# Performance work log

Measured on AMD Instinct MI355X. Metric: run time of the kernel, lower is better.

Reference implementation:

```python
import jax, jax.numpy as jnp
import numpy as np

N, E, D, R, L = 50000, 800000, 128, 4, 2


def setup_inputs() -> dict:
    key = jax.random.key(0)
    ks = jax.random.split(key, 6)
    x = jax.random.normal(ks[0], (N, D), dtype=jnp.float32)
    edge_index = jax.random.randint(ks[1], (2, E), 0, N, dtype=jnp.int64)
    edge_type = jax.random.randint(ks[2], (E,), 0, R, dtype=jnp.int64)
    # per-layer params: relation weights, root weights, biases (fan-in scaled)
    weights = jax.random.normal(ks[3], (L, R, D, D), dtype=jnp.float32) / np.sqrt(D)
    roots = jax.random.normal(ks[4], (L, D, D), dtype=jnp.float32) / np.sqrt(D)
    biases = jnp.zeros((L, D), dtype=jnp.float32)
    return {"x": x, "edge_index": edge_index, "edge_type": edge_type,
            "weights": weights, "roots": roots, "biases": biases}


def _rgcn_conv(x, src, dst, edge_type, weight, root, bias):
    # x: [N, D_in]; weight: [R, D_in, D_out]; root: [D_in, D_out]; bias: [D_out]
    out = x @ root + bias  # root/self transform
    for r in range(R):  # small fixed relation count
        h = x @ weight[r]                                   # [N, D_out]
        m = (edge_type == r).astype(h.dtype)                # [E]
        msgs = h[src] * m[:, None]                          # [E, D_out] gathered messages
        agg = jax.ops.segment_sum(msgs, dst, num_segments=N)
        cnt = jax.ops.segment_sum(m, dst, num_segments=N)
        out = out + agg / jnp.maximum(cnt, 1.0)[:, None]    # per-relation scatter-mean
    return out


def reference(x, edge_index, edge_type, weights, roots, biases):
    src, dst = edge_index[0], edge_index[1]
    h = x
    for i in range(L):
        h = _rgcn_conv(h, src, dst, edge_type, weights[i], roots[i], biases[i])
        if i != L - 1:
            h = jax.nn.relu(h)
    return h
```

## Files before the change

kernel.cpp:

```cpp
#include <hip/hip_runtime.h>


#define N_NODES 50000
#define N_EDGES 800000
#define N_REL 4
#define DIM 128
#define NPAD 50048
#define RN (N_REL * N_NODES)
#define CAP 32

#define HIST_B 3125
#define XCAST_B 3125
#define WPREP_B 640
#define PREP_B (HIST_B + XCAST_B + WPREP_B)

typedef __bf16 bf16x8 __attribute__((ext_vector_type(8)));
typedef float f32x4 __attribute__((ext_vector_type(4)));
typedef float f32x2 __attribute__((ext_vector_type(2)));

__device__ __forceinline__ unsigned short f2bf(float f) {
    unsigned u = __builtin_bit_cast(unsigned, f);
    u += 0x7FFFu + ((u >> 16) & 1u);
    return (unsigned short)(u >> 16);
}

__device__ __forceinline__ unsigned cvt_pk_bf16(float lo, float hi) {
    unsigned r;
    asm("v_cvt_pk_bf16_f32 %0, %1, %2" : "=v"(r) : "v"(lo), "v"(hi));
    return r;
}

__device__ __forceinline__ void pk_add(f32x2& acc, f32x2 v) {
    asm("v_pk_add_f32 %0, %1, %0" : "+v"(acc) : "v"(v));
}

__device__ __forceinline__ void acc_row(f32x2* acc, uint4 d) {
#pragma unroll
    for (int k = 0; k < 4; k++) {
        unsigned dw = (&d.x)[k];
        f32x2 v;
        v[0] = __builtin_bit_cast(float, dw << 16);
        v[1] = __builtin_bit_cast(float, dw & 0xFFFF0000u);
        pk_add(acc[k], v);
    }
}

__device__ __forceinline__ void gload_lds16(const void* g, void* lds) {
    __builtin_amdgcn_global_load_lds(
        (const __attribute__((address_space(1))) void*)g,
        (__attribute__((address_space(3))) void*)lds, 16, 0, 0);
}

__global__ __launch_bounds__(256) void k_prep(const int* __restrict__ et,
                                              const int* __restrict__ dst,
                                              const int* __restrict__ src,
                                              int* __restrict__ cnt,
                                              unsigned short* __restrict__ elist,
                                              const float* __restrict__ X,
                                              unsigned short* __restrict__ Xb,
                                              const float* __restrict__ weights,
                                              const float* __restrict__ roots,
                                              unsigned short* __restrict__ wcatT) {
    const int blk = blockIdx.x, tid = threadIdx.x;
    if (blk < HIST_B) {
        int i = blk * 256 + tid;
        int rn = (dst[i] << 2) | et[i];
        int rk = atomicAdd(&cnt[rn], 1);
        if (rk < CAP) elist[(size_t)rn * CAP + rk] = (unsigned short)src[i];
    } else if (blk < HIST_B + XCAST_B) {
        int i = (blk - HIST_B) * 256 + tid;
        f32x4 a = *(const f32x4*)(X + (size_t)i * 8);
        f32x4 b = *(const f32x4*)(X + (size_t)i * 8 + 4);
        uint4 o;
        o.x = cvt_pk_bf16(a[0], a[1]);
        o.y = cvt_pk_bf16(a[2], a[3]);
        o.z = cvt_pk_bf16(b[0], b[1]);
        o.w = cvt_pk_bf16(b[2], b[3]);
        *(uint4*)(Xb + (size_t)i * 8) = o;
    } else {
        int idx = (blk - HIST_B - XCAST_B) * 256 + tid;
        int k = idx % 640;
        int n = (idx / 640) % 128;
        int l = idx / (640 * 128);
        float v;
        if (k < 128) {
            v = roots[(l * 128 + k) * 128 + n];
        } else {
            int r = (k - 128) >> 7;
            int kk = (k - 128) & 127;
            v = weights[((l * N_REL + r) * 128 + kk) * 128 + n];
        }
        wcatT[idx] = f2bf(v);
    }
}

__global__ __launch_bounds__(256) void k_agg(const unsigned short* __restrict__ Xb,
                                             const int* __restrict__ cnt,
                                             const unsigned short* __restrict__ elist,
                                             unsigned short* __restrict__ xcat) {
    int node = blockIdx.x * 4 + (threadIdx.x >> 6);
    int lane = threadIdx.x & 63;
    const int g = lane >> 4;
    const int t = lane & 15;

    int bucket = (node << 2) | g;
    int c = cnt[bucket];
    c = (c > CAP) ? CAP : c;
    const unsigned short* ep = elist + ((size_t)bucket * CAP);
    uint4 e8 = *(const uint4*)ep;

    int i0 = e8.x & 0xFFFF, i1 = e8.x >> 16;
    int i2 = e8.y & 0xFFFF, i3 = e8.y >> 16;
    int i4 = e8.z & 0xFFFF, i5 = e8.z >> 16;
    int i6 = e8.w & 0xFFFF, i7 = e8.w >> 16;

    const size_t toff = (size_t)(t * 8);
    const uint4 z = {0, 0, 0, 0};
    f32x2 A0[4] = {}, A1[4] = {}, A2[4] = {}, A3[4] = {};

    {
        uint4 d0 = z, d1 = z, d2 = z, d3 = z;
        if (c > 0) d0 = *(const uint4*)(Xb + (size_t)i0 * DIM + toff);
        if (c > 1) d1 = *(const uint4*)(Xb + (size_t)i1 * DIM + toff);
        if (c > 2) d2 = *(const uint4*)(Xb + (size_t)i2 * DIM + toff);
        if (c > 3) d3 = *(const uint4*)(Xb + (size_t)i3 * DIM + toff);
        acc_row(A0, d0); acc_row(A1, d1); acc_row(A2, d2); acc_row(A3, d3);
    }
    if (c > 4) {
        uint4 d0 = z, d1 = z, d2 = z, d3 = z;
        d0 = *(const uint4*)(Xb + (size_t)i4 * DIM + toff);
        if (c > 5) d1 = *(const uint4*)(Xb + (size_t)i5 * DIM + toff);
        if (c > 6) d2 = *(const uint4*)(Xb + (size_t)i6 * DIM + toff);
        if (c > 7) d3 = *(const uint4*)(Xb + (size_t)i7 * DIM + toff);
        acc_row(A0, d0); acc_row(A1, d1); acc_row(A2, d2); acc_row(A3, d3);
    }
    for (int j = 8; j < c; ++j) {
        int s = ep[j];
        uint4 d = *(const uint4*)(Xb + (size_t)s * DIM + toff);
        acc_row(A0, d);
    }
#pragma unroll
    for (int k = 0; k < 4; k++) {
        pk_add(A0[k], A1[k]);
        pk_add(A2[k], A3[k]);
        pk_add(A0[k], A2[k]);
    }

    float inv = 1.0f / fmaxf((float)c, 1.0f);
    uint4 o;
    o.x = cvt_pk_bf16(A0[0][0] * inv, A0[0][1] * inv);
    o.y = cvt_pk_bf16(A0[1][0] * inv, A0[1][1] * inv);
    o.z = cvt_pk_bf16(A0[2][0] * inv, A0[2][1] * inv);
    o.w = cvt_pk_bf16(A0[3][0] * inv, A0[3][1] * inv);
    *(uint4*)(xcat + (size_t)node * 512 + g * 128 + t * 8) = o;
}

__global__ __launch_bounds__(256) void k_gemm(const unsigned short* __restrict__ Xself,
                                              const unsigned short* __restrict__ Xagg,
                                              const unsigned short* __restrict__ Bt,
                                              const float* __restrict__ bias,
                                              void* __restrict__ Yv, int Mout,
                                              int relu, int obf16) {
    __shared__ unsigned short sA[64 * 64];
    __shared__ unsigned short sB[128 * 64];

    const int tid = threadIdx.x;
    const int lane = tid & 63;
    const int wid = tid >> 6;
    const int wm = wid >> 1, wn = wid & 1;
    const int m0 = blockIdx.x * 64;

    f32x4 acc[2][4] = {};

    const char* Bbase = (const char*)Bt;

    for (int kt = 0; kt < 10; ++kt) {
        const char* Asrc;
        size_t rstride;
        if (kt < 2) {
            Asrc = (const char*)Xself + (size_t)m0 * 256 + kt * 128;
            rstride = 256;
        } else {
            Asrc = (const char*)Xagg + (size_t)m0 * 1024 + (kt - 2) * 128;
            rstride = 1024;
        }
#pragma unroll
        for (int i = 0; i < 2; i++) {
            int chunk = i * 256 + tid;
            int row = chunk >> 3, cst = chunk & 7;
            int clog = cst ^ (row & 7);
            gload_lds16(Asrc + (size_t)row * rstride + clog * 16,
                        (char*)sA + (size_t)(chunk - lane) * 16);
        }
#pragma unroll
        for (int i = 0; i < 4; i++) {
            int chunk = i * 256 + tid;
            int row = chunk >> 3, cst = chunk & 7;
            int clog = cst ^ (row & 7);
            gload_lds16(Bbase + (size_t)row * 1280 + kt * 128 + clog * 16,
                        (char*)sB + (size_t)(chunk - lane) * 16);
        }
        __syncthreads();
#pragma unroll
        for (int ki = 0; ki < 2; ki++) {
            bf16x8 a[2], b[4];
#pragma unroll
            for (int mi = 0; mi < 2; mi++) {
                int row = wm * 32 + mi * 16 + (lane & 15);
                int c = ki * 4 + (lane >> 4);
                a[mi] = *(const bf16x8*)((const char*)sA + row * 128 + ((c ^ (row & 7)) << 4));
            }
#pragma unroll
            for (int ni = 0; ni < 4; ni++) {
                int row = wn * 64 + ni * 16 + (lane & 15);
                int c = ki * 4 + (lane >> 4);
                b[ni] = *(const bf16x8*)((const char*)sB + row * 128 + ((c ^ (row & 7)) << 4));
            }
#pragma unroll
            for (int mi = 0; mi < 2; mi++)
#pragma unroll
                for (int ni = 0; ni < 4; ni++)
                    acc[mi][ni] = __builtin_amdgcn_mfma_f32_16x16x32_bf16(a[mi], b[ni], acc[mi][ni], 0, 0, 0);
        }
        __syncthreads();
    }
#pragma unroll
    for (int mi = 0; mi < 2; mi++) {
#pragma unroll
        for (int ni = 0; ni < 4; ni++) {
            int col = wn * 64 + ni * 16 + (lane & 15);
            float bv = bias[col];
#pragma unroll
            for (int q = 0; q < 4; q++) {
                int row = m0 + wm * 32 + mi * 16 + (lane >> 4) * 4 + q;
                if (row < Mout) {
                    float v = acc[mi][ni][q] + bv;
                    if (relu) v = fmaxf(v, 0.f);
                    if (obf16)
                        ((unsigned short*)Yv)[(size_t)row * DIM + col] = f2bf(v);
                    else
                        ((float*)Yv)[(size_t)row * DIM + col] = v;
                }
            }
        }
    }
}

extern "C" void kernel_launch(void* const* d_in, const int* in_sizes, int n_in,
                              void* d_out, int out_size, void* d_ws, size_t ws_size,
                              hipStream_t stream) {
    const float* x = (const float*)d_in[0];
    const int* ei = (const int*)d_in[1];
    const int* et = (const int*)d_in[2];
    const float* weights = (const float*)d_in[3];
    const float* roots = (const float*)d_in[4];
    const float* biases = (const float*)d_in[5];
    float* out = (float*)d_out;

    const int* src = ei;
    const int* dst = ei + N_EDGES;

    int* cnt = (int*)d_ws;
    unsigned short* elist = (unsigned short*)(cnt + 200064);
    unsigned short* wcatT = elist + (size_t)RN * CAP;
    unsigned short* xcat = wcatT + 2 * 128 * 640;
    unsigned short* xb = xcat + (size_t)NPAD * 512;
    unsigned short* hb = xb + (size_t)NPAD * 128;

    hipMemsetAsync(cnt, 0, (size_t)200064 * sizeof(int), stream);

    k_prep<<<PREP_B, 256, 0, stream>>>(et, dst, src, cnt, elist, x, xb, weights, roots, wcatT);

    k_agg<<<N_NODES / 4, 256, 0, stream>>>(xb, cnt, elist, xcat);
    k_gemm<<<NPAD / 64, 256, 0, stream>>>(xb, xcat, wcatT, biases, hb, N_NODES, 1, 1);
    k_agg<<<N_NODES / 4, 256, 0, stream>>>(hb, cnt, elist, xcat);
    k_gemm<<<NPAD / 64, 256, 0, stream>>>(hb, xcat, wcatT + 128 * 640, biases + DIM, out, N_NODES, 0, 0);
}
```

Before: 168.5 us.

## Partition histogram by XCD dst range, widen gather to 8 loads, nontemporal stores

The edge histogram kernel is reorganised so that each block is tied to an XCD (blk&7) and handles only edges whose destination falls in that XCD's node range. Every edge chunk is therefore scanned by 8 blocks, but the atomics and elist writes stay local to one XCD's L2. The aggregation kernel now issues all 8 first-edge gathers up front into 8 independent accumulators, for more memory-level parallelism. The aggregated output and the final fp32 GEMM output use nontemporal stores. The trade-off is that dst is read 8 times over, and the XCD mapping assumes round-robin block dispatch.

```diff
diff --git a/kernel.cpp b/kernel.cpp
--- a/kernel.cpp
+++ b/kernel.cpp
@@ -8,8 +8,11 @@
 #define NPAD 50048
 #define RN (N_REL * N_NODES)
 #define CAP 32
-
-#define HIST_B 3125
+#define NXCD 8
+#define DRANGE 6250
+
+#define HIST_G 391
+#define HIST_B (HIST_G * NXCD)
 #define XCAST_B 3125
 #define WPREP_B 640
 #define PREP_B (HIST_B + XCAST_B + WPREP_B)
@@ -17,6 +20,7 @@
 typedef __bf16 bf16x8 __attribute__((ext_vector_type(8)));
 typedef float f32x4 __attribute__((ext_vector_type(4)));
 typedef float f32x2 __attribute__((ext_vector_type(2)));
+typedef unsigned int u32x4 __attribute__((ext_vector_type(4)));
 
 __device__ __forceinline__ unsigned short f2bf(float f) {
     unsigned u = __builtin_bit_cast(unsigned, f);
@@ -63,20 +67,32 @@
                                               unsigned short* __restrict__ wcatT) {
     const int blk = blockIdx.x, tid = threadIdx.x;
     if (blk < HIST_B) {
-        int i = blk * 256 + tid;
-        int rn = (dst[i] << 2) | et[i];
-        int rk = atomicAdd(&cnt[rn], 1);
-        if (rk < CAP) elist[(size_t)rn * CAP + rk] = (unsigned short)src[i];
+        const int g = blk >> 3;
+        const int x = blk & 7;
+        const int lo = x * DRANGE, hi = lo + DRANGE;
+        const int base = g * 2048;
+#pragma unroll
+        for (int j = 0; j < 8; j++) {
+            int i = base + j * 256 + tid;
+            if (i < N_EDGES) {
+                int d = dst[i];
+                if (d >= lo && d < hi) {
+                    int rn = (d << 2) | et[i];
+                    int rk = atomicAdd(&cnt[rn], 1);
+                    if (rk < CAP) elist[(size_t)rn * CAP + rk] = (unsigned short)src[i];
+                }
+            }
+        }
     } else if (blk < HIST_B + XCAST_B) {
         int i = (blk - HIST_B) * 256 + tid;
         f32x4 a = *(const f32x4*)(X + (size_t)i * 8);
         f32x4 b = *(const f32x4*)(X + (size_t)i * 8 + 4);
-        uint4 o;
+        u32x4 o;
         o.x = cvt_pk_bf16(a[0], a[1]);
         o.y = cvt_pk_bf16(a[2], a[3]);
         o.z = cvt_pk_bf16(b[0], b[1]);
         o.w = cvt_pk_bf16(b[2], b[3]);
-        *(uint4*)(Xb + (size_t)i * 8) = o;
+        *(u32x4*)(Xb + (size_t)i * 8) = o;
     } else {
         int idx = (blk - HIST_B - XCAST_B) * 256 + tid;
         int k = idx % 640;
@@ -117,22 +133,20 @@
     const size_t toff = (size_t)(t * 8);
     const uint4 z = {0, 0, 0, 0};
     f32x2 A0[4] = {}, A1[4] = {}, A2[4] = {}, A3[4] = {};
+    f32x2 A4[4] = {}, A5[4] = {}, A6[4] = {}, A7[4] = {};
 
     {
-        uint4 d0 = z, d1 = z, d2 = z, d3 = z;
+        uint4 d0 = z, d1 = z, d2 = z, d3 = z, d4 = z, d5 = z, d6 = z, d7 = z;
         if (c > 0) d0 = *(const uint4*)(Xb + (size_t)i0 * DIM + toff);
         if (c > 1) d1 = *(const uint4*)(Xb + (size_t)i1 * DIM + toff);
         if (c > 2) d2 = *(const uint4*)(Xb + (size_t)i2 * DIM + toff);
         if (c > 3) d3 = *(const uint4*)(Xb + (size_t)i3 * DIM + toff);
+        if (c > 4) d4 = *(const uint4*)(Xb + (size_t)i4 * DIM + toff);
+        if (c > 5) d5 = *(const uint4*)(Xb + (size_t)i5 * DIM + toff);
+        if (c > 6) d6 = *(const uint4*)(Xb + (size_t)i6 * DIM + toff);
+        if (c > 7) d7 = *(const uint4*)(Xb + (size_t)i7 * DIM + toff);
         acc_row(A0, d0); acc_row(A1, d1); acc_row(A2, d2); acc_row(A3, d3);
-    }
-    if (c > 4) {
-        uint4 d0 = z, d1 = z, d2 = z, d3 = z;
-        d0 = *(const uint4*)(Xb + (size_t)i4 * DIM + toff);
-        if (c > 5) d1 = *(const uint4*)(Xb + (size_t)i5 * DIM + toff);
-        if (c > 6) d2 = *(const uint4*)(Xb + (size_t)i6 * DIM + toff);
-        if (c > 7) d3 = *(const uint4*)(Xb + (size_t)i7 * DIM + toff);
-        acc_row(A0, d0); acc_row(A1, d1); acc_row(A2, d2); acc_row(A3, d3);
+        acc_row(A4, d4); acc_row(A5, d5); acc_row(A6, d6); acc_row(A7, d7);
     }
     for (int j = 8; j < c; ++j) {
         int s = ep[j];
@@ -143,16 +157,20 @@
     for (int k = 0; k < 4; k++) {
         pk_add(A0[k], A1[k]);
         pk_add(A2[k], A3[k]);
+        pk_add(A4[k], A5[k]);
+        pk_add(A6[k], A7[k]);
         pk_add(A0[k], A2[k]);
+        pk_add(A4[k], A6[k]);
+        pk_add(A0[k], A4[k]);
     }
 
     float inv = 1.0f / fmaxf((float)c, 1.0f);
-    uint4 o;
+    u32x4 o;
     o.x = cvt_pk_bf16(A0[0][0] * inv, A0[0][1] * inv);
     o.y = cvt_pk_bf16(A0[1][0] * inv, A0[1][1] * inv);
     o.z = cvt_pk_bf16(A0[2][0] * inv, A0[2][1] * inv);
     o.w = cvt_pk_bf16(A0[3][0] * inv, A0[3][1] * inv);
-    *(uint4*)(xcat + (size_t)node * 512 + g * 128 + t * 8) = o;
+    __builtin_nontemporal_store(o, (u32x4*)(xcat + (size_t)node * 512 + g * 128 + t * 8));
 }
 
 __global__ __launch_bounds__(256) void k_gemm(const unsigned short* __restrict__ Xself,
@@ -236,10 +254,11 @@
                 if (row < Mout) {
                     float v = acc[mi][ni][q] + bv;
                     if (relu) v = fmaxf(v, 0.f);
-                    if (obf16)
+                    if (obf16) {
                         ((unsigned short*)Yv)[(size_t)row * DIM + col] = f2bf(v);
-                    else
-                        ((float*)Yv)[(size_t)row * DIM + col] = v;
+                    } else {
+                        __builtin_nontemporal_store(v, (float*)Yv + (size_t)row * DIM + col);
+                    }
                 }
             }
         }
```

New measurement: 213.3 us. 26.6% more time.

## Pack bucket counts into bytes and split edge lists into dense head plus overflow

Applied to the files above, without the earlier changes.

Edge-bucket counters become 8-bit fields packed four to a 32-bit word, so one atomic word serves all four relations of a node and the memset shrinks fourfold. The per-bucket source lists split into a dense 8-entry head array and a separate 24-entry overflow array. The aggregation kernel then reads a compact 16-byte head per bucket instead of touching a 64-byte-stride list, which cuts scattered memory traffic and the workspace footprint. Counts above 255 would wrap the byte field, so correctness depends on per-bucket degree staying small, which holds for these random inputs.

```diff
diff --git a/kernel.cpp b/kernel.cpp
--- a/kernel.cpp
+++ b/kernel.cpp
@@ -8,6 +8,7 @@
 #define NPAD 50048
 #define RN (N_REL * N_NODES)
 #define CAP 32
+#define OVF 24
 
 #define HIST_B 3125
 #define XCAST_B 3125
@@ -17,6 +18,7 @@
 typedef __bf16 bf16x8 __attribute__((ext_vector_type(8)));
 typedef float f32x4 __attribute__((ext_vector_type(4)));
 typedef float f32x2 __attribute__((ext_vector_type(2)));
+typedef unsigned int u32x4 __attribute__((ext_vector_type(4)));
 
 __device__ __forceinline__ unsigned short f2bf(float f) {
     unsigned u = __builtin_bit_cast(unsigned, f);
@@ -54,8 +56,9 @@
 __global__ __launch_bounds__(256) void k_prep(const int* __restrict__ et,
                                               const int* __restrict__ dst,
                                               const int* __restrict__ src,
-                                              int* __restrict__ cnt,
-                                              unsigned short* __restrict__ elist,
+                                              unsigned* __restrict__ cnt32,
+                                              unsigned short* __restrict__ elist8,
+                                              unsigned short* __restrict__ ovf,
                                               const float* __restrict__ X,
                                               unsigned short* __restrict__ Xb,
                                               const float* __restrict__ weights,
@@ -65,18 +68,24 @@
     if (blk < HIST_B) {
         int i = blk * 256 + tid;
         int rn = (dst[i] << 2) | et[i];
-        int rk = atomicAdd(&cnt[rn], 1);
-        if (rk < CAP) elist[(size_t)rn * CAP + rk] = (unsigned short)src[i];
+        int sh = 8 * (rn & 3);
+        unsigned old = atomicAdd(&cnt32[rn >> 2], 1u << sh);
+        int rk = (old >> sh) & 0xFF;
+        if (rk < 8) {
+            elist8[(size_t)rn * 8 + rk] = (unsigned short)src[i];
+        } else if (rk < CAP) {
+            ovf[(size_t)rn * OVF + (rk - 8)] = (unsigned short)src[i];
+        }
     } else if (blk < HIST_B + XCAST_B) {
         int i = (blk - HIST_B) * 256 + tid;
         f32x4 a = *(const f32x4*)(X + (size_t)i * 8);
         f32x4 b = *(const f32x4*)(X + (size_t)i * 8 + 4);
-        uint4 o;
+        u32x4 o;
         o.x = cvt_pk_bf16(a[0], a[1]);
         o.y = cvt_pk_bf16(a[2], a[3]);
         o.z = cvt_pk_bf16(b[0], b[1]);
         o.w = cvt_pk_bf16(b[2], b[3]);
-        *(uint4*)(Xb + (size_t)i * 8) = o;
+        *(u32x4*)(Xb + (size_t)i * 8) = o;
     } else {
         int idx = (blk - HIST_B - XCAST_B) * 256 + tid;
         int k = idx % 640;
@@ -95,8 +104,9 @@
 }
 
 __global__ __launch_bounds__(256) void k_agg(const unsigned short* __restrict__ Xb,
-                                             const int* __restrict__ cnt,
-                                             const unsigned short* __restrict__ elist,
+                                             const unsigned char* __restrict__ cnt8,
+                                             const unsigned short* __restrict__ elist8,
+                                             const unsigned short* __restrict__ ovf,
                                              unsigned short* __restrict__ xcat) {
     int node = blockIdx.x * 4 + (threadIdx.x >> 6);
     int lane = threadIdx.x & 63;
@@ -104,10 +114,9 @@
     const int t = lane & 15;
 
     int bucket = (node << 2) | g;
-    int c = cnt[bucket];
+    int c = cnt8[bucket];
     c = (c > CAP) ? CAP : c;
-    const unsigned short* ep = elist + ((size_t)bucket * CAP);
-    uint4 e8 = *(const uint4*)ep;
+    uint4 e8 = *(const uint4*)(elist8 + (size_t)bucket * 8);
 
     int i0 = e8.x & 0xFFFF, i1 = e8.x >> 16;
     int i2 = e8.y & 0xFFFF, i3 = e8.y >> 16;
@@ -135,7 +144,7 @@
         acc_row(A0, d0); acc_row(A1, d1); acc_row(A2, d2); acc_row(A3, d3);
     }
     for (int j = 8; j < c; ++j) {
-        int s = ep[j];
+        int s = ovf[(size_t)bucket * OVF + (j - 8)];
         uint4 d = *(const uint4*)(Xb + (size_t)s * DIM + toff);
         acc_row(A0, d);
     }
@@ -147,12 +156,12 @@
     }
 
     float inv = 1.0f / fmaxf((float)c, 1.0f);
-    uint4 o;
+    u32x4 o;
     o.x = cvt_pk_bf16(A0[0][0] * inv, A0[0][1] * inv);
     o.y = cvt_pk_bf16(A0[1][0] * inv, A0[1][1] * inv);
     o.z = cvt_pk_bf16(A0[2][0] * inv, A0[2][1] * inv);
     o.w = cvt_pk_bf16(A0[3][0] * inv, A0[3][1] * inv);
-    *(uint4*)(xcat + (size_t)node * 512 + g * 128 + t * 8) = o;
+    *(u32x4*)(xcat + (size_t)node * 512 + g * 128 + t * 8) = o;
 }
 
 __global__ __launch_bounds__(256) void k_gemm(const unsigned short* __restrict__ Xself,
@@ -260,19 +269,21 @@
     const int* src = ei;
     const int* dst = ei + N_EDGES;
 
-    int* cnt = (int*)d_ws;
-    unsigned short* elist = (unsigned short*)(cnt + 200064);
-    unsigned short* wcatT = elist + (size_t)RN * CAP;
+    unsigned* cnt32 = (unsigned*)d_ws;
+    unsigned short* elist8 = (unsigned short*)(cnt32 + 50016);
+    unsigned short* ovf = elist8 + (size_t)RN * 8;
+    unsigned short* wcatT = ovf + (size_t)RN * OVF;
     unsigned short* xcat = wcatT + 2 * 128 * 640;
     unsigned short* xb = xcat + (size_t)NPAD * 512;
     unsigned short* hb = xb + (size_t)NPAD * 128;
 
-    hipMemsetAsync(cnt, 0, (size_t)200064 * sizeof(int), stream);
-
-    k_prep<<<PREP_B, 256, 0, stream>>>(et, dst, src, cnt, elist, x, xb, weights, roots, wcatT);
-
-    k_agg<<<N_NODES / 4, 256, 0, stream>>>(xb, cnt, elist, xcat);
+    hipMemsetAsync(cnt32, 0, (size_t)50016 * sizeof(unsigned), stream);
+
+    k_prep<<<PREP_B, 256, 0, stream>>>(et, dst, src, cnt32, elist8, ovf, x, xb,
+                                       weights, roots, wcatT);
+
+    k_agg<<<N_NODES / 4, 256, 0, stream>>>(xb, (const unsigned char*)cnt32, elist8, ovf, xcat);
     k_gemm<<<NPAD / 64, 256, 0, stream>>>(xb, xcat, wcatT, biases, hb, N_NODES, 1, 1);
-    k_agg<<<N_NODES / 4, 256, 0, stream>>>(hb, cnt, elist, xcat);
+    k_agg<<<N_NODES / 4, 256, 0, stream>>>(hb, (const unsigned char*)cnt32, elist8, ovf, xcat);
     k_gemm<<<NPAD / 64, 256, 0, stream>>>(hb, xcat, wcatT + 128 * 640, biases + DIM, out, N_NODES, 0, 0);
 }
```

Result: no change. 170.2 us (+1.0%).
